# Kernel optimization log

Measured on AMD Instinct MI355X. Metric: run time of the kernel, lower is better.

The kernel has to match this reference:

```python
import jax, jax.numpy as jnp
import numpy as np

N_NODES = 100000
N_EDGES = 500000
D_IN = 128
D_HID = 256
D_OUT = 1


def mish(x):
    # x * tanh(softplus(x))
    return x * jnp.tanh(jax.nn.softplus(x))


def setup_inputs() -> dict:
    key = jax.random.key(0)
    k1, k2, k3, k4, k5, k6 = jax.random.split(key, 6)
    z = jax.random.normal(k1, (N_NODES, D_IN), dtype=jnp.float32)
    edge = jax.random.randint(k2, (2, N_EDGES), 0, N_NODES, dtype=jnp.int64)
    # PyTorch Linear default init: U(-1/sqrt(fan_in), 1/sqrt(fan_in))
    s1 = 1.0 / np.sqrt(D_IN)
    s2 = 1.0 / np.sqrt(D_HID)
    W1 = jax.random.uniform(k3, (D_HID, D_IN), minval=-s1, maxval=s1, dtype=jnp.float32)
    b1 = jax.random.uniform(k4, (D_HID,), minval=-s1, maxval=s1, dtype=jnp.float32)
    W2 = jax.random.uniform(k5, (D_OUT, D_HID), minval=-s2, maxval=s2, dtype=jnp.float32)
    b2 = jax.random.uniform(k6, (D_OUT,), minval=-s2, maxval=s2, dtype=jnp.float32)
    return {"z": z, "edge": edge, "W1": W1, "b1": b1, "W2": W2, "b2": b2}


def reference(z, edge, W1, b1, W2, b2):
    # gather node pairs and elementwise product: [E, D_IN]
    x = z[edge[0]] * z[edge[1]]
    # fc1 + mish (dropout is identity in eval mode)
    h = mish(jnp.einsum('ed,hd->eh', x, W1) + b1)
    # fc2 + sigmoid -> [E, 1]
    logits = jnp.einsum('eh,oh->eo', h, W2) + b2
    return jax.nn.sigmoid(logits)
```

## Files before the change

### kernel.cpp

```cpp
#include <hip/hip_runtime.h>
#include <hip/hip_bf16.h>


#define N_EDGES 500000
#define D_IN    128
#define D_HID   256
#define M_TILE  32
#define NTILES  (N_EDGES / M_TILE)
#define LDS_STRIDE 136
#define GRID    512

typedef __bf16 bf16x8 __attribute__((ext_vector_type(8)));
typedef float  f32x4  __attribute__((ext_vector_type(4)));
typedef float  f32x2  __attribute__((ext_vector_type(2)));

union F4H { float4 v; f32x2 h[2]; };

__device__ __forceinline__ unsigned int pkbf(f32x2 q) {
    union { __hip_bfloat162 b; unsigned int u; } c;
    c.b = __float22bfloat162_rn(make_float2(q.x, q.y));
    return c.u;
}

__device__ __forceinline__ f32x2 mish2(f32x2 x) {
    f32x2 xc = {fminf(x.x, 20.0f), fminf(x.y, 20.0f)};
    f32x2 E  = {__expf(xc.x), __expf(xc.y)};
    f32x2 num = E * (E + 2.0f);
    f32x2 den = num + 2.0f;
    f32x2 r  = {__builtin_amdgcn_rcpf(den.x), __builtin_amdgcn_rcpf(den.y)};
    return x * num * r;
}

__global__ __launch_bounds__(512, 4)
void edge_decoder_kernel(const float* __restrict__ z,
                         const int*   __restrict__ edge,
                         const float* __restrict__ W1,
                         const float* __restrict__ b1,
                         const float* __restrict__ W2,
                         const float* __restrict__ b2,
                         float*       __restrict__ out) {
    __shared__ ushort xbuf[2][M_TILE * LDS_STRIDE];
    __shared__ float  lpart[2][8][M_TILE];

    const int t    = threadIdx.x;
    const int wave = t >> 6;
    const int lane = t & 63;
    const int quad = lane >> 4;
    const int nlo  = lane & 15;

    bf16x8 bfrag[4][2];
    float  b1f[2], w2f[2];
    #pragma unroll
    for (int nt = 0; nt < 2; ++nt) {
        const int n = wave * 32 + nt * 16 + nlo;
        const float* wrow = W1 + n * D_IN;
        #pragma unroll
        for (int ks = 0; ks < 4; ++ks) {
            F4H w0, w1;
            w0.v = *reinterpret_cast<const float4*>(wrow + ks * 32 + quad * 8);
            w1.v = *reinterpret_cast<const float4*>(wrow + ks * 32 + quad * 8 + 4);
            union { unsigned int u[4]; bf16x8 v; } o;
            o.u[0] = pkbf(w0.h[0]); o.u[1] = pkbf(w0.h[1]);
            o.u[2] = pkbf(w1.h[0]); o.u[3] = pkbf(w1.h[1]);
            bfrag[ks][nt] = o.v;
        }
        b1f[nt] = b1[n];
        w2f[nt] = W2[n];
    }
    const float b2f = b2[0];

    const int s_slot = t >> 4;
    const int cch    = t & 15;

    int tile = blockIdx.x;
    float4 a0, a1, c0, c1;
    {
        const int e = tile * M_TILE + s_slot;
        const int u = edge[e], v = edge[N_EDGES + e];
        const float* zu = z + (size_t)u * D_IN + cch * 8;
        const float* zv = z + (size_t)v * D_IN + cch * 8;
        a0 = *reinterpret_cast<const float4*>(zu);
        a1 = *reinterpret_cast<const float4*>(zu + 4);
        c0 = *reinterpret_cast<const float4*>(zv);
        c1 = *reinterpret_cast<const float4*>(zv + 4);
    }
    int u_n, v_n;
    {
        const int t1 = min(tile + GRID, NTILES - 1);
        const int e1 = t1 * M_TILE + s_slot;
        u_n = edge[e1]; v_n = edge[N_EDGES + e1];
    }

    int  p = 0;
    bool have_prev = false;
    int  prev_base = 0;

    for (; tile < NTILES; tile += GRID) {
        {
            F4H A0{a0}, A1{a1}, C0{c0}, C1{c1};
            unsigned int r0 = pkbf(A0.h[0] * C0.h[0]);
            unsigned int r1 = pkbf(A0.h[1] * C0.h[1]);
            unsigned int r2 = pkbf(A1.h[0] * C1.h[0]);
            unsigned int r3 = pkbf(A1.h[1] * C1.h[1]);
            *reinterpret_cast<uint4*>(&xbuf[p][s_slot * LDS_STRIDE + cch * 8]) =
                make_uint4(r0, r1, r2, r3);
        }
        __syncthreads();

        {
            const float* zu = z + (size_t)u_n * D_IN + cch * 8;
            const float* zv = z + (size_t)v_n * D_IN + cch * 8;
            a0 = *reinterpret_cast<const float4*>(zu);
            a1 = *reinterpret_cast<const float4*>(zu + 4);
            c0 = *reinterpret_cast<const float4*>(zv);
            c1 = *reinterpret_cast<const float4*>(zv + 4);
        }
        {
            const int t2 = min(tile + 2 * GRID, NTILES - 1);
            const int e2 = t2 * M_TILE + s_slot;
            u_n = edge[e2]; v_n = edge[N_EDGES + e2];
        }

        if (have_prev) {
            if (t < M_TILE) {
                const int pp = p ^ 1;
                float logit = b2f;
                #pragma unroll
                for (int w = 0; w < 8; ++w) logit += lpart[pp][w][t];
                out[prev_base + t] = __builtin_amdgcn_rcpf(1.0f + __expf(-logit));
            }
        }

        f32x4 acc[2][2];
        #pragma unroll
        for (int mt = 0; mt < 2; ++mt)
            #pragma unroll
            for (int nt = 0; nt < 2; ++nt)
                acc[mt][nt] = (f32x4){0.f, 0.f, 0.f, 0.f};

        #pragma unroll
        for (int ks = 0; ks < 4; ++ks) {
            bf16x8 af[2];
            #pragma unroll
            for (int mt = 0; mt < 2; ++mt)
                af[mt] = *reinterpret_cast<const bf16x8*>(
                    &xbuf[p][(mt * 16 + nlo) * LDS_STRIDE + ks * 32 + quad * 8]);
            #pragma unroll
            for (int mt = 0; mt < 2; ++mt)
                #pragma unroll
                for (int nt = 0; nt < 2; ++nt)
                    acc[mt][nt] = __builtin_amdgcn_mfma_f32_16x16x32_bf16(
                        af[mt], bfrag[ks][nt], acc[mt][nt], 0, 0, 0);
        }

        #pragma unroll
        for (int mt = 0; mt < 2; ++mt) {
            #pragma unroll
            for (int pr = 0; pr < 2; ++pr) {
                f32x2 s2 = {0.f, 0.f};
                #pragma unroll
                for (int nt = 0; nt < 2; ++nt) {
                    f32x2 h = {acc[mt][nt][2 * pr]     + b1f[nt],
                               acc[mt][nt][2 * pr + 1] + b1f[nt]};
                    f32x2 m = mish2(h);
                    s2.x += m.x * w2f[nt];
                    s2.y += m.y * w2f[nt];
                }
                float sx = s2.x, sy = s2.y;
                sx += __shfl_xor(sx, 1); sy += __shfl_xor(sy, 1);
                sx += __shfl_xor(sx, 2); sy += __shfl_xor(sy, 2);
                sx += __shfl_xor(sx, 4); sy += __shfl_xor(sy, 4);
                sx += __shfl_xor(sx, 8); sy += __shfl_xor(sy, 8);
                if (nlo == 0) {
                    const int row = mt * 16 + quad * 4 + pr * 2;
                    lpart[p][wave][row]     = sx;
                    lpart[p][wave][row + 1] = sy;
                }
            }
        }

        have_prev = true;
        prev_base = tile * M_TILE;
        p ^= 1;
    }

    __syncthreads();
    if (have_prev && t < M_TILE) {
        const int pp = p ^ 1;
        float logit = b2f;
        #pragma unroll
        for (int w = 0; w < 8; ++w) logit += lpart[pp][w][t];
        out[prev_base + t] = __builtin_amdgcn_rcpf(1.0f + __expf(-logit));
    }
}

extern "C" void kernel_launch(void* const* d_in, const int* in_sizes, int n_in,
                              void* d_out, int out_size, void* d_ws, size_t ws_size,
                              hipStream_t stream) {
    const float* z    = (const float*)d_in[0];
    const int*   edge = (const int*)d_in[1];
    const float* W1   = (const float*)d_in[2];
    const float* b1   = (const float*)d_in[3];
    const float* W2   = (const float*)d_in[4];
    const float* b2   = (const float*)d_in[5];
    float* out = (float*)d_out;

    edge_decoder_kernel<<<dim3(GRID), dim3(512), 0, stream>>>(z, edge, W1, b1, W2, b2, out);
}
```

Baseline: 177.7 us.

## Pre-convert node features to bf16 in workspace and gather half-width rows

Adds a pre-pass kernel that converts z to bf16 in the workspace. The edge kernel then gathers 16-byte bf16 rows instead of 32-byte fp32 rows, halving the random-gather traffic. It also doubles the persistent grid size. The cost is an extra full pass over z (read 51MB, write 25MB) and one extra rounding of the inputs before the product.

```diff
diff --git a/kernel.cpp b/kernel.cpp
--- a/kernel.cpp
+++ b/kernel.cpp
@@ -2,13 +2,14 @@
 #include <hip/hip_bf16.h>
 
 
+#define N_NODES 100000
 #define N_EDGES 500000
 #define D_IN    128
 #define D_HID   256
 #define M_TILE  32
 #define NTILES  (N_EDGES / M_TILE)
 #define LDS_STRIDE 136
-#define GRID    512
+#define GRID    1024
 
 typedef __bf16 bf16x8 __attribute__((ext_vector_type(8)));
 typedef float  f32x4  __attribute__((ext_vector_type(4)));
@@ -20,6 +21,12 @@
     union { __hip_bfloat162 b; unsigned int u; } c;
     c.b = __float22bfloat162_rn(make_float2(q.x, q.y));
     return c.u;
+}
+__device__ __forceinline__ float bflo(unsigned int w) {
+    union { unsigned int u; float f; } c; c.u = w << 16; return c.f;
+}
+__device__ __forceinline__ float bfhi(unsigned int w) {
+    union { unsigned int u; float f; } c; c.u = w & 0xffff0000u; return c.f;
 }
 
 __device__ __forceinline__ f32x2 mish2(f32x2 x) {
@@ -31,14 +38,25 @@
     return x * num * r;
 }
 
+__global__ __launch_bounds__(256)
+void z_to_bf16(const float* __restrict__ z, ushort* __restrict__ zb) {
+    const int i = (blockIdx.x * 256 + threadIdx.x) * 8;
+    F4H a{*reinterpret_cast<const float4*>(z + i)};
+    F4H b{*reinterpret_cast<const float4*>(z + i + 4)};
+    *reinterpret_cast<uint4*>(zb + i) =
+        make_uint4(pkbf(a.h[0]), pkbf(a.h[1]), pkbf(b.h[0]), pkbf(b.h[1]));
+}
+
+template<bool ZBF>
 __global__ __launch_bounds__(512, 4)
-void edge_decoder_kernel(const float* __restrict__ z,
-                         const int*   __restrict__ edge,
-                         const float* __restrict__ W1,
-                         const float* __restrict__ b1,
-                         const float* __restrict__ W2,
-                         const float* __restrict__ b2,
-                         float*       __restrict__ out) {
+void edge_decoder_kernel(const float*  __restrict__ zf,
+                         const ushort* __restrict__ zb,
+                         const int*    __restrict__ edge,
+                         const float*  __restrict__ W1,
+                         const float*  __restrict__ b1,
+                         const float*  __restrict__ W2,
+                         const float*  __restrict__ b2,
+                         float*        __restrict__ out) {
     __shared__ ushort xbuf[2][M_TILE * LDS_STRIDE];
     __shared__ float  lpart[2][8][M_TILE];
 
@@ -56,9 +74,8 @@
         const float* wrow = W1 + n * D_IN;
         #pragma unroll
         for (int ks = 0; ks < 4; ++ks) {
-            F4H w0, w1;
-            w0.v = *reinterpret_cast<const float4*>(wrow + ks * 32 + quad * 8);
-            w1.v = *reinterpret_cast<const float4*>(wrow + ks * 32 + quad * 8 + 4);
+            F4H w0{*reinterpret_cast<const float4*>(wrow + ks * 32 + quad * 8)};
+            F4H w1{*reinterpret_cast<const float4*>(wrow + ks * 32 + quad * 8 + 4)};
             union { unsigned int u[4]; bf16x8 v; } o;
             o.u[0] = pkbf(w0.h[0]); o.u[1] = pkbf(w0.h[1]);
             o.u[2] = pkbf(w1.h[0]); o.u[3] = pkbf(w1.h[1]);
@@ -73,16 +90,22 @@
     const int cch    = t & 15;
 
     int tile = blockIdx.x;
+    uint4  ua, va;
     float4 a0, a1, c0, c1;
     {
         const int e = tile * M_TILE + s_slot;
         const int u = edge[e], v = edge[N_EDGES + e];
-        const float* zu = z + (size_t)u * D_IN + cch * 8;
-        const float* zv = z + (size_t)v * D_IN + cch * 8;
-        a0 = *reinterpret_cast<const float4*>(zu);
-        a1 = *reinterpret_cast<const float4*>(zu + 4);
-        c0 = *reinterpret_cast<const float4*>(zv);
-        c1 = *reinterpret_cast<const float4*>(zv + 4);
+        if constexpr (ZBF) {
+            ua = *reinterpret_cast<const uint4*>(zb + (size_t)u * D_IN + cch * 8);
+            va = *reinterpret_cast<const uint4*>(zb + (size_t)v * D_IN + cch * 8);
+        } else {
+            const float* zu = zf + (size_t)u * D_IN + cch * 8;
+            const float* zv = zf + (size_t)v * D_IN + cch * 8;
+            a0 = *reinterpret_cast<const float4*>(zu);
+            a1 = *reinterpret_cast<const float4*>(zu + 4);
+            c0 = *reinterpret_cast<const float4*>(zv);
+            c1 = *reinterpret_cast<const float4*>(zv + 4);
+        }
     }
     int u_n, v_n;
     {
@@ -96,20 +119,32 @@
     int  prev_base = 0;
 
     for (; tile < NTILES; tile += GRID) {
-        {
+        if constexpr (ZBF) {
+            unsigned int uu[4] = {ua.x, ua.y, ua.z, ua.w};
+            unsigned int vv[4] = {va.x, va.y, va.z, va.w};
+            unsigned int r[4];
+            #pragma unroll
+            for (int j = 0; j < 4; ++j) {
+                f32x2 fu = {bflo(uu[j]), bfhi(uu[j])};
+                f32x2 fv = {bflo(vv[j]), bfhi(vv[j])};
+                r[j] = pkbf(fu * fv);
+            }
+            *reinterpret_cast<uint4*>(&xbuf[p][s_slot * LDS_STRIDE + cch * 8]) =
+                make_uint4(r[0], r[1], r[2], r[3]);
+        } else {
             F4H A0{a0}, A1{a1}, C0{c0}, C1{c1};
-            unsigned int r0 = pkbf(A0.h[0] * C0.h[0]);
-            unsigned int r1 = pkbf(A0.h[1] * C0.h[1]);
-            unsigned int r2 = pkbf(A1.h[0] * C1.h[0]);
-            unsigned int r3 = pkbf(A1.h[1] * C1.h[1]);
             *reinterpret_cast<uint4*>(&xbuf[p][s_slot * LDS_STRIDE + cch * 8]) =
-                make_uint4(r0, r1, r2, r3);
+                make_uint4(pkbf(A0.h[0] * C0.h[0]), pkbf(A0.h[1] * C0.h[1]),
+                           pkbf(A1.h[0] * C1.h[0]), pkbf(A1.h[1] * C1.h[1]));
         }
         __syncthreads();
 
-        {
-            const float* zu = z + (size_t)u_n * D_IN + cch * 8;
-            const float* zv = z + (size_t)v_n * D_IN + cch * 8;
+        if constexpr (ZBF) {
+            ua = *reinterpret_cast<const uint4*>(zb + (size_t)u_n * D_IN + cch * 8);
+            va = *reinterpret_cast<const uint4*>(zb + (size_t)v_n * D_IN + cch * 8);
+        } else {
+            const float* zu = zf + (size_t)u_n * D_IN + cch * 8;
+            const float* zv = zf + (size_t)v_n * D_IN + cch * 8;
             a0 = *reinterpret_cast<const float4*>(zu);
             a1 = *reinterpret_cast<const float4*>(zu + 4);
             c0 = *reinterpret_cast<const float4*>(zv);
@@ -121,14 +156,12 @@
             u_n = edge[e2]; v_n = edge[N_EDGES + e2];
         }
 
-        if (have_prev) {
-            if (t < M_TILE) {
-                const int pp = p ^ 1;
-                float logit = b2f;
-                #pragma unroll
-                for (int w = 0; w < 8; ++w) logit += lpart[pp][w][t];
-                out[prev_base + t] = __builtin_amdgcn_rcpf(1.0f + __expf(-logit));
-            }
+        if (have_prev && t < M_TILE) {
+            const int pp = p ^ 1;
+            float logit = b2f;
+            #pragma unroll
+            for (int w = 0; w < 8; ++w) logit += lpart[pp][w][t];
+            out[prev_base + t] = __builtin_amdgcn_rcpf(1.0f + __expf(-logit));
         }
 
         f32x4 acc[2][2];
@@ -205,5 +238,14 @@
     const float* b2   = (const float*)d_in[5];
     float* out = (float*)d_out;
 
-    edge_decoder_kernel<<<dim3(GRID), dim3(512), 0, stream>>>(z, edge, W1, b1, W2, b2, out);
-}
+    const size_t zb_bytes = (size_t)N_NODES * D_IN * sizeof(ushort);
+    if (ws_size >= zb_bytes) {
+        ushort* zb = (ushort*)d_ws;
+        z_to_bf16<<<dim3((N_NODES * D_IN) / (256 * 8)), dim3(256), 0, stream>>>(z, zb);
+        edge_decoder_kernel<true><<<dim3(GRID), dim3(512), 0, stream>>>(
+            z, zb, edge, W1, b1, W2, b2, out);
+    } else {
+        edge_decoder_kernel<false><<<dim3(GRID), dim3(512), 0, stream>>>(
+            z, nullptr, edge, W1, b1, W2, b2, out);
+    }
+}
```

Result: slower. 186.5 us (+5.0%).

## Swap GEMM operands to 32x32x16 MFMA with weights as A and double grid

Applied to the files above, without the earlier changes.

Switches the per-tile hidden-layer GEMM from four 16x16x32 MFMAs per k-step to one 32x32x16 MFMA per k-step. W1 now sits in the A operand and the edge features in B, so each lane's output column is one edge. The layer-2 reduction across hidden units then happens mostly in registers and needs one cross-half shuffle instead of a four-step shuffle tree. The bias is folded into the accumulator initialisation, and the grid is doubled to 1024 blocks to give more concurrency for the gather-bound loads. It adds more accumulator and bias/w2 registers per thread, which may reduce occupancy under the 512x4 launch bounds.

```diff
diff --git a/kernel.cpp b/kernel.cpp
--- a/kernel.cpp
+++ b/kernel.cpp
@@ -8,10 +8,10 @@
 #define M_TILE  32
 #define NTILES  (N_EDGES / M_TILE)
 #define LDS_STRIDE 136
-#define GRID    512
+#define GRID    1024
 
 typedef __bf16 bf16x8 __attribute__((ext_vector_type(8)));
-typedef float  f32x4  __attribute__((ext_vector_type(4)));
+typedef float  f32x16 __attribute__((ext_vector_type(16)));
 typedef float  f32x2  __attribute__((ext_vector_type(2)));
 
 union F4H { float4 v; f32x2 h[2]; };
@@ -45,27 +45,29 @@
     const int t    = threadIdx.x;
     const int wave = t >> 6;
     const int lane = t & 63;
-    const int quad = lane >> 4;
-    const int nlo  = lane & 15;
+    const int half = lane >> 5;
+    const int col  = lane & 31;
 
-    bf16x8 bfrag[4][2];
-    float  b1f[2], w2f[2];
-    #pragma unroll
-    for (int nt = 0; nt < 2; ++nt) {
-        const int n = wave * 32 + nt * 16 + nlo;
-        const float* wrow = W1 + n * D_IN;
+    bf16x8 afragW[8];
+    {
+        const float* wrow = W1 + (size_t)(wave * 32 + col) * D_IN;
         #pragma unroll
-        for (int ks = 0; ks < 4; ++ks) {
-            F4H w0, w1;
-            w0.v = *reinterpret_cast<const float4*>(wrow + ks * 32 + quad * 8);
-            w1.v = *reinterpret_cast<const float4*>(wrow + ks * 32 + quad * 8 + 4);
+        for (int kk = 0; kk < 8; ++kk) {
+            const float* wp = wrow + kk * 16 + half * 8;
+            F4H w0{*reinterpret_cast<const float4*>(wp)};
+            F4H w1{*reinterpret_cast<const float4*>(wp + 4)};
             union { unsigned int u[4]; bf16x8 v; } o;
             o.u[0] = pkbf(w0.h[0]); o.u[1] = pkbf(w0.h[1]);
             o.u[2] = pkbf(w1.h[0]); o.u[3] = pkbf(w1.h[1]);
-            bfrag[ks][nt] = o.v;
+            afragW[kk] = o.v;
         }
-        b1f[nt] = b1[n];
-        w2f[nt] = W2[n];
+    }
+    float b1c[16], w2f[16];
+    #pragma unroll
+    for (int r = 0; r < 16; ++r) {
+        const int n = wave * 32 + (r & 3) + 8 * (r >> 2) + 4 * half;
+        b1c[r] = b1[n];
+        w2f[r] = W2[n];
     }
     const float b2f = b2[0];
 
@@ -98,12 +100,9 @@
     for (; tile < NTILES; tile += GRID) {
         {
             F4H A0{a0}, A1{a1}, C0{c0}, C1{c1};
-            unsigned int r0 = pkbf(A0.h[0] * C0.h[0]);
-            unsigned int r1 = pkbf(A0.h[1] * C0.h[1]);
-            unsigned int r2 = pkbf(A1.h[0] * C1.h[0]);
-            unsigned int r3 = pkbf(A1.h[1] * C1.h[1]);
             *reinterpret_cast<uint4*>(&xbuf[p][s_slot * LDS_STRIDE + cch * 8]) =
-                make_uint4(r0, r1, r2, r3);
+                make_uint4(pkbf(A0.h[0] * C0.h[0]), pkbf(A0.h[1] * C0.h[1]),
+                           pkbf(A1.h[0] * C1.h[0]), pkbf(A1.h[1] * C1.h[1]));
         }
         __syncthreads();
 
@@ -121,63 +120,35 @@
             u_n = edge[e2]; v_n = edge[N_EDGES + e2];
         }
 
-        if (have_prev) {
-            if (t < M_TILE) {
-                const int pp = p ^ 1;
-                float logit = b2f;
-                #pragma unroll
-                for (int w = 0; w < 8; ++w) logit += lpart[pp][w][t];
-                out[prev_base + t] = __builtin_amdgcn_rcpf(1.0f + __expf(-logit));
-            }
+        if (have_prev && t < M_TILE) {
+            const int pp = p ^ 1;
+            float logit = b2f;
+            #pragma unroll
+            for (int w = 0; w < 8; ++w) logit += lpart[pp][w][t];
+            out[prev_base + t] = __builtin_amdgcn_rcpf(1.0f + __expf(-logit));
         }
 
-        f32x4 acc[2][2];
+        f32x16 acc;
         #pragma unroll
-        for (int mt = 0; mt < 2; ++mt)
-            #pragma unroll
-            for (int nt = 0; nt < 2; ++nt)
-                acc[mt][nt] = (f32x4){0.f, 0.f, 0.f, 0.f};
+        for (int r = 0; r < 16; ++r) acc[r] = b1c[r];
 
         #pragma unroll
-        for (int ks = 0; ks < 4; ++ks) {
-            bf16x8 af[2];
-            #pragma unroll
-            for (int mt = 0; mt < 2; ++mt)
-                af[mt] = *reinterpret_cast<const bf16x8*>(
-                    &xbuf[p][(mt * 16 + nlo) * LDS_STRIDE + ks * 32 + quad * 8]);
-            #pragma unroll
-            for (int mt = 0; mt < 2; ++mt)
-                #pragma unroll
-                for (int nt = 0; nt < 2; ++nt)
-                    acc[mt][nt] = __builtin_amdgcn_mfma_f32_16x16x32_bf16(
-                        af[mt], bfrag[ks][nt], acc[mt][nt], 0, 0, 0);
+        for (int kk = 0; kk < 8; ++kk) {
+            bf16x8 bx = *reinterpret_cast<const bf16x8*>(
+                &xbuf[p][col * LDS_STRIDE + kk * 16 + half * 8]);
+            acc = __builtin_amdgcn_mfma_f32_32x32x16_bf16(afragW[kk], bx, acc, 0, 0, 0);
         }
 
+        float s = 0.f;
         #pragma unroll
-        for (int mt = 0; mt < 2; ++mt) {
-            #pragma unroll
-            for (int pr = 0; pr < 2; ++pr) {
-                f32x2 s2 = {0.f, 0.f};
-                #pragma unroll
-                for (int nt = 0; nt < 2; ++nt) {
-                    f32x2 h = {acc[mt][nt][2 * pr]     + b1f[nt],
-                               acc[mt][nt][2 * pr + 1] + b1f[nt]};
-                    f32x2 m = mish2(h);
-                    s2.x += m.x * w2f[nt];
-                    s2.y += m.y * w2f[nt];
-                }
-                float sx = s2.x, sy = s2.y;
-                sx += __shfl_xor(sx, 1); sy += __shfl_xor(sy, 1);
-                sx += __shfl_xor(sx, 2); sy += __shfl_xor(sy, 2);
-                sx += __shfl_xor(sx, 4); sy += __shfl_xor(sy, 4);
-                sx += __shfl_xor(sx, 8); sy += __shfl_xor(sy, 8);
-                if (nlo == 0) {
-                    const int row = mt * 16 + quad * 4 + pr * 2;
-                    lpart[p][wave][row]     = sx;
-                    lpart[p][wave][row + 1] = sy;
-                }
-            }
+        for (int r = 0; r < 16; r += 2) {
+            f32x2 h = {acc[r], acc[r + 1]};
+            f32x2 m = mish2(h);
+            s = fmaf(m.x, w2f[r], s);
+            s = fmaf(m.y, w2f[r + 1], s);
         }
+        s += __shfl_xor(s, 32);
+        if (lane < 32) lpart[p][wave][col] = s;
 
         have_prev = true;
         prev_base = tile * M_TILE;
```

After: 262.2 us. 1.48x slower.
